# Kernel optimization log

Measured on AMD Instinct MI355X. Metric: run time of the kernel, lower is better.

## Reference

```python
import jax, jax.numpy as jnp
import numpy as np

N_NODES = 100000
N_EDGES = 1250000
D_IN = 64
D_OUT = 64


def setup_inputs() -> dict:
    key = jax.random.key(0)
    k1, k2, k3, k4, k5 = jax.random.split(key, 5)
    x = jax.random.normal(k1, (N_NODES, D_IN), dtype=jnp.float32)
    edge_index = jax.random.randint(k2, (2, N_EDGES), 0, N_NODES, dtype=jnp.int64)
    # Linear weights stored torch-style as [out, in]
    w_neigh = jax.random.normal(k3, (D_OUT, D_IN), dtype=jnp.float32) / np.sqrt(D_IN)
    w_self = jax.random.normal(k4, (D_OUT, D_IN), dtype=jnp.float32) / np.sqrt(D_IN)
    b_self = jax.random.normal(k5, (D_OUT,), dtype=jnp.float32) * 0.01
    return {"x": x, "edge_index": edge_index, "w_neigh": w_neigh, "w_self": w_self, "b_self": b_self}


def reference(x, edge_index, w_neigh, w_self, b_self):
    num_nodes = x.shape[0]
    src, dst = edge_index[0], edge_index[1]
    # mean aggregation of neighbor features: scatter-add then divide by in-degree
    agg = jax.ops.segment_sum(x[src], dst, num_segments=num_nodes)  # [N, d]
    degree = jax.ops.segment_sum(jnp.ones_like(dst, dtype=x.dtype), dst, num_segments=num_nodes)
    degree = jnp.maximum(degree, 1.0)
    agg = agg / degree[:, None]
    return agg @ w_neigh.T + x @ w_self.T + b_self
```

## Files before the change

### kernel.cpp

```cpp
#include <hip/hip_runtime.h>

#define N_NODES 100000
#define N_EDGES 1250000
#define D 64
#define BSH 6
#define BNODES 64
#define NB 1563
#define WSW 68
#define G 512
#define CHUNK 2444
#define MM_BLOCKS ((N_NODES + 127) / 128)
#define BIN_BLOCKS 128
#define BIN_CHUNK ((N_EDGES + BIN_BLOCKS - 1) / BIN_BLOCKS)

typedef unsigned int u32;
typedef short bf16x8 __attribute__((ext_vector_type(8)));
typedef float f32x4 __attribute__((ext_vector_type(4)));

__device__ __forceinline__ u32 pack_bf16(float lo, float hi) {
    u32 a = __float_as_uint(lo);
    u32 b = __float_as_uint(hi);
    a = (a + 0x7fffu + ((a >> 16) & 1u)) >> 16;
    b = (b + 0x7fffu + ((b >> 16) & 1u)) >> 16;
    return a | (b << 16);
}

__global__ void __launch_bounds__(256) k_histw(const int* __restrict__ ei,
                                               u32* __restrict__ ghist,
                                               const float* __restrict__ wn,
                                               const float* __restrict__ wsf,
                                               u32* __restrict__ bfrag) {
    __shared__ u32 hist[NB];
    int tid = threadIdx.x;
    if (blockIdx.x < G) {
        int g = blockIdx.x;
        int e0 = g * CHUNK, e1 = min(e0 + CHUNK, N_EDGES);
        for (int i = tid; i < NB; i += 256) hist[i] = 0;
        __syncthreads();
        const int4* dp = (const int4*)(ei + N_EDGES + e0);
        int nv = (e1 - e0) >> 2;
        for (int i = tid; i < nv; i += 256) {
            int4 d4 = dp[i];
            atomicAdd(&hist[d4.x >> BSH], 1u);
            atomicAdd(&hist[d4.y >> BSH], 1u);
            atomicAdd(&hist[d4.z >> BSH], 1u);
            atomicAdd(&hist[d4.w >> BSH], 1u);
        }
        __syncthreads();
        for (int i = tid; i < NB; i += 256)
            ghist[(size_t)i * G + g] = hist[i];
    } else {
        for (int i = tid; i < 4096; i += 256) {
            int t = i >> 9, h = (i >> 8) & 1, l = (i >> 2) & 63, q = i & 3;
            int k0 = h * 32 + (l >> 4) * 8 + 2 * q;
            int n = t * 16 + (l & 15);
            const float* w = (n < 64) ? &wn[(size_t)n * 64] : &wsf[(size_t)(n - 64) * 64];
            bfrag[i] = pack_bf16(w[k0], w[k0 + 1]);
        }
    }
}

__global__ void __launch_bounds__(512) k_scanB(const u32* __restrict__ ghist,
                                               u32* __restrict__ gbase,
                                               u32* __restrict__ bcnt) {
    __shared__ u32 wt[8];
    int t = threadIdx.x;
    int b = blockIdx.x;
    int lane = t & 63, wv = t >> 6;
    u32 v = ghist[(size_t)b * G + t];
    u32 s = v;
#pragma unroll
    for (int off = 1; off < 64; off <<= 1) {
        u32 n = __shfl_up(s, off, 64);
        if (lane >= off) s += n;
    }
    if (lane == 63) wt[wv] = s;
    __syncthreads();
    u32 add = 0;
#pragma unroll
    for (int q = 0; q < 8; ++q) add += (q < wv) ? wt[q] : 0u;
    u32 incl = s + add;
    gbase[(size_t)b * G + t] = incl - v;
    if (t == G - 1) bcnt[b] = incl;
}

__global__ void __launch_bounds__(256) k_scatmm(const int* __restrict__ ei,
                                                const u32* __restrict__ gbase,
                                                u32* __restrict__ binned,
                                                int cap,
                                                const float* __restrict__ x,
                                                const u32* __restrict__ bfrag,
                                                const float* __restrict__ bias,
                                                u32* __restrict__ y16,
                                                float* __restrict__ zout) {
    __shared__ u32 cur[NB];
    int tid = threadIdx.x;
    if (blockIdx.x < G) {
        int g = blockIdx.x;
        int e0 = g * CHUNK, e1 = min(e0 + CHUNK, N_EDGES);
        for (int i = tid; i < NB; i += 256)
            cur[i] = gbase[(size_t)i * G + g];
        __syncthreads();
        const int4* sp = (const int4*)(ei + e0);
        const int4* dp = (const int4*)(ei + N_EDGES + e0);
        int nv = (e1 - e0) >> 2;
        for (int i = tid; i < nv; i += 256) {
            int4 s4 = sp[i];
            int4 d4 = dp[i];
            int ss[4] = {s4.x, s4.y, s4.z, s4.w};
            int dd[4] = {d4.x, d4.y, d4.z, d4.w};
#pragma unroll
            for (int u = 0; u < 4; ++u) {
                int b = dd[u] >> BSH;
                u32 loc = atomicAdd(&cur[b], 1u);
                if (loc < (u32)cap)
                    binned[(size_t)b * cap + loc] = ((u32)ss[u] << BSH) | (u32)(dd[u] & (BNODES - 1));
            }
        }
        return;
    }

    int w = tid >> 6, l = tid & 63;
    int lg = l >> 4, c = l & 15;
    int nodebase = (blockIdx.x - G) * 128 + w * 32;

    union FU { uint4 u; bf16x8 v; };

    bf16x8 af[2][2];
#pragma unroll
    for (int m = 0; m < 2; ++m) {
        int node = nodebase + m * 16 + c;
        if (node >= N_NODES) node = N_NODES - 1;
        const float4* xr = (const float4*)(x + (size_t)node * D);
#pragma unroll
        for (int h = 0; h < 2; ++h) {
            float4 p0 = xr[h * 8 + lg * 2];
            float4 p1 = xr[h * 8 + lg * 2 + 1];
            FU au;
            au.u.x = pack_bf16(p0.x, p0.y);
            au.u.y = pack_bf16(p0.z, p0.w);
            au.u.z = pack_bf16(p1.x, p1.y);
            au.u.w = pack_bf16(p1.z, p1.w);
            af[m][h] = au.v;
        }
    }

    f32x4 acc[2][8];
#pragma unroll
    for (int m = 0; m < 2; ++m) {
#pragma unroll
        for (int t = 0; t < 4; ++t) acc[m][t] = (f32x4){0.f, 0.f, 0.f, 0.f};
#pragma unroll
        for (int t = 4; t < 8; ++t) {
            float bb = bias[(t - 4) * 16 + c];
            acc[m][t] = (f32x4){bb, bb, bb, bb};
        }
    }

    const uint4* bp = (const uint4*)bfrag;
#pragma unroll
    for (int tc = 0; tc < 2; ++tc) {
        bf16x8 bf[4][2];
#pragma unroll
        for (int tt = 0; tt < 4; ++tt)
#pragma unroll
            for (int h = 0; h < 2; ++h) {
                FU bu;
                bu.u = bp[(((tc * 4 + tt) * 2 + h) * 64) + l];
                bf[tt][h] = bu.v;
            }
#pragma unroll
        for (int m = 0; m < 2; ++m)
#pragma unroll
            for (int tt = 0; tt < 4; ++tt) {
                int t = tc * 4 + tt;
                acc[m][t] = __builtin_amdgcn_mfma_f32_16x16x32_bf16(
                    af[m][0], bf[tt][0], acc[m][t], 0, 0, 0);
                acc[m][t] = __builtin_amdgcn_mfma_f32_16x16x32_bf16(
                    af[m][1], bf[tt][1], acc[m][t], 0, 0, 0);
            }
    }

#pragma unroll
    for (int m = 0; m < 2; ++m) {
        int rowbase = nodebase + m * 16 + lg * 4;
#pragma unroll
        for (int r = 0; r < 4; ++r) {
            int node = rowbase + r;
            bool ok = node < N_NODES;
#pragma unroll
            for (int t = 4; t < 8; ++t) {
                if (ok) zout[(size_t)node * D + (t - 4) * 16 + c] = acc[m][t][r];
            }
#pragma unroll
            for (int t = 0; t < 4; ++t) {
                float v = acc[m][t][r];
                float o = __shfl_xor(v, 1);
                if (ok && !(c & 1))
                    y16[(size_t)node * 32 + t * 8 + (c >> 1)] = pack_bf16(v, o);
            }
        }
    }
}

__global__ void __launch_bounds__(256) k_sort(u32* __restrict__ binned,
                                              const u32* __restrict__ bcnt,
                                              int cap,
                                              uint2* __restrict__ meta) {
    __shared__ u32 eh[1024];
    __shared__ u32 hist[BNODES];
    __shared__ u32 cur[BNODES];
    int tid = threadIdx.x;
    int b = blockIdx.x;
    int cnt = min((int)bcnt[b], cap);
    u32* seg = binned + (size_t)b * cap;

    if (tid < BNODES) hist[tid] = 0;
    __syncthreads();
    const uint4* segv = (const uint4*)seg;
    int nv = cnt >> 2;
    for (int i = tid; i < nv; i += 256) {
        uint4 w4 = segv[i];
        *(uint4*)&eh[4 * i] = w4;
        atomicAdd(&hist[w4.x & (BNODES - 1)], 1u);
        atomicAdd(&hist[w4.y & (BNODES - 1)], 1u);
        atomicAdd(&hist[w4.z & (BNODES - 1)], 1u);
        atomicAdd(&hist[w4.w & (BNODES - 1)], 1u);
    }
    for (int i = (cnt & ~3) + tid; i < cnt; i += 256) {
        u32 w = seg[i];
        eh[i] = w;
        atomicAdd(&hist[w & (BNODES - 1)], 1u);
    }
    __syncthreads();
    if (tid < BNODES) {
        u32 v = hist[tid];
        u32 s = v;
#pragma unroll
        for (int off = 1; off < 64; off <<= 1) {
            u32 n = __shfl_up(s, off, 64);
            if (tid >= off) s += n;
        }
        u32 excl = s - v;
        cur[tid] = excl;
        int node = (b << BSH) + tid;
        if (node < N_NODES)
            meta[node] = make_uint2((u32)((size_t)b * cap + excl), v);
    }
    __syncthreads();
    for (int i = tid; i < cnt; i += 256) {
        u32 w = eh[i];
        u32 p = atomicAdd(&cur[w & (BNODES - 1)], 1u);
        seg[p] = w >> BSH;
    }
}

__global__ void __launch_bounds__(256) k_gather_yz(const u32* __restrict__ y16,
                                                   const u32* __restrict__ binned,
                                                   const uint2* __restrict__ meta,
                                                   float* __restrict__ io) {
    int tid = blockIdx.x * 256 + threadIdx.x;
    int node = tid >> 6;
    if (node >= N_NODES) return;
    int lane = threadIdx.x & 63;
    int sub = lane >> 4;
    int pr = lane & 15;
    const uint2* yv = (const uint2*)y16;
    uint2 m = meta[node];
    u32 o0 = m.x, dg = m.y;

    u32 myidx = 0;
    if (lane < (int)dg) myidx = binned[o0 + lane];

    float a0 = 0.f, a1 = 0.f, a2 = 0.f, a3 = 0.f;
    u32 dmain = min(dg, 64u);
    for (u32 r = 0; r < dmain; r += 32) {
        uint2 w[8];
#pragma unroll
        for (int t = 0; t < 8; ++t) {
            u32 e = r + 4 * t + sub;
            u32 idx = (u32)__shfl((int)myidx, (int)(e & 63));
            w[t] = make_uint2(0u, 0u);
            if (e < dmain) w[t] = yv[(size_t)idx * 16 + pr];
        }
#pragma unroll
        for (int t = 0; t < 8; ++t) {
            if (r + 4u * (u32)t < dmain) {
                a0 += __uint_as_float(w[t].x << 16);
                a1 += __uint_as_float(w[t].x & 0xffff0000u);
                a2 += __uint_as_float(w[t].y << 16);
                a3 += __uint_as_float(w[t].y & 0xffff0000u);
            }
        }
    }
    for (u32 j = o0 + 64; j < o0 + dg; j += 16) {
#pragma unroll
        for (int t = 0; t < 4; ++t) {
            u32 ie = j + 4 * t + sub;
            if (ie < o0 + dg) {
                u32 idx = binned[ie];
                uint2 w = yv[(size_t)idx * 16 + pr];
                a0 += __uint_as_float(w.x << 16);
                a1 += __uint_as_float(w.x & 0xffff0000u);
                a2 += __uint_as_float(w.y << 16);
                a3 += __uint_as_float(w.y & 0xffff0000u);
            }
        }
    }

    a0 += __shfl_xor(a0, 16); a1 += __shfl_xor(a1, 16);
    a2 += __shfl_xor(a2, 16); a3 += __shfl_xor(a3, 16);
    a0 += __shfl_xor(a0, 32); a1 += __shfl_xor(a1, 32);
    a2 += __shfl_xor(a2, 32); a3 += __shfl_xor(a3, 32);
    if (sub == 0) {
        float inv = 1.0f / (float)max(dg, 1u);
        float4 z = *(const float4*)&io[(size_t)node * D + 4 * pr];
        *(float4*)&io[(size_t)node * D + 4 * pr] =
            make_float4(z.x + a0 * inv, z.y + a1 * inv, z.z + a2 * inv, z.w + a3 * inv);
    }
}

__global__ void __launch_bounds__(256) k_bin2(const int* __restrict__ ei,
                                              u32* __restrict__ bcnt,
                                              u32* __restrict__ binned,
                                              int cap) {
    __shared__ u32 hist[NB];
    __shared__ u32 rbase[NB];
    int tid = threadIdx.x;
    int e0 = blockIdx.x * BIN_CHUNK;
    int e1 = min(e0 + BIN_CHUNK, N_EDGES);
    const int* dstp = ei + N_EDGES;
    for (int i = tid; i < NB; i += 256) hist[i] = 0;
    __syncthreads();
    for (int e = e0 + tid; e < e1; e += 256)
        atomicAdd(&hist[dstp[e] >> BSH], 1u);
    __syncthreads();
    for (int i = tid; i < NB; i += 256) {
        u32 h = hist[i];
        rbase[i] = h ? atomicAdd(&bcnt[i], h) : 0u;
        hist[i] = 0;
    }
    __syncthreads();
    for (int e = e0 + tid; e < e1; e += 256) {
        int d = dstp[e];
        int s = ei[e];
        int b = d >> BSH;
        u32 loc = atomicAdd(&hist[b], 1u);
        u32 slot = rbase[b] + loc;
        if (slot < (u32)cap)
            binned[(size_t)b * cap + slot] = ((u32)s << BSH) | (u32)(d & (BNODES - 1));
    }
}

__global__ void __launch_bounds__(256) k_sort_fb(u32* __restrict__ binned,
                                                 const u32* __restrict__ bcnt,
                                                 int cap,
                                                 u32* __restrict__ offs,
                                                 u32* __restrict__ deg) {
    __shared__ u32 eh[1024];
    __shared__ u32 hist[BNODES];
    __shared__ u32 cur[BNODES];
    int tid = threadIdx.x;
    int b = blockIdx.x;
    int cnt = min((int)bcnt[b], cap);
    u32* seg = binned + (size_t)b * cap;
    if (tid < BNODES) hist[tid] = 0;
    __syncthreads();
    for (int i = tid; i < cnt; i += 256) {
        u32 w = seg[i];
        eh[i] = w;
        atomicAdd(&hist[w & (BNODES - 1)], 1u);
    }
    __syncthreads();
    if (tid < BNODES) {
        u32 v = hist[tid];
        u32 s = v;
#pragma unroll
        for (int off = 1; off < 64; off <<= 1) {
            u32 n = __shfl_up(s, off, 64);
            if (tid >= off) s += n;
        }
        u32 excl = s - v;
        cur[tid] = excl;
        int node = (b << BSH) + tid;
        if (node < N_NODES) {
            offs[node] = (u32)((size_t)b * cap + excl);
            deg[node] = v;
        }
    }
    __syncthreads();
    for (int i = tid; i < cnt; i += 256) {
        u32 w = eh[i];
        u32 p = atomicAdd(&cur[w & (BNODES - 1)], 1u);
        seg[p] = w >> BSH;
    }
}

__global__ void __launch_bounds__(256) k_gather32(const float* __restrict__ x,
                                                  const u32* __restrict__ binned,
                                                  const u32* __restrict__ offs,
                                                  const u32* __restrict__ deg,
                                                  float* __restrict__ agg) {
    int tid = blockIdx.x * 256 + threadIdx.x;
    int node = tid >> 6;
    int d = tid & 63;
    if (node >= N_NODES) return;
    u32 o0 = offs[node], dg = deg[node];
    u32 o1 = o0 + dg;
    float s = 0.f;
    u32 j = o0;
    for (; j + 8 <= o1; j += 8) {
        u32 e[8];
        float v[8];
#pragma unroll
        for (int t = 0; t < 8; ++t) e[t] = binned[j + t];
#pragma unroll
        for (int t = 0; t < 8; ++t) v[t] = x[(size_t)e[t] * D + d];
#pragma unroll
        for (int t = 0; t < 8; ++t) s += v[t];
    }
    for (; j < o1; ++j) s += x[(size_t)binned[j] * D + d];
    agg[(size_t)node * D + d] = s / (float)max(dg, 1u);
}

__global__ void __launch_bounds__(256) k_gemm_fb(const float* __restrict__ x,
                                                 const float* __restrict__ wn,
                                                 const float* __restrict__ wsf,
                                                 const float* __restrict__ bias,
                                                 float* __restrict__ io) {
    __shared__ float At[BNODES * WSW];
    __shared__ float Wt[128 * WSW];
    int tid = threadIdx.x;
    int base = blockIdx.x * 64;
    const float4* iop = (const float4*)io;
    const float4* xp  = (const float4*)x;
    for (int i = tid; i < 4096; i += 256) {
        int d = i >> 6, k = i & 63;
        Wt[k * WSW + d] = wn[i];
        Wt[(64 + k) * WSW + d] = wsf[i];
    }
    for (int i = tid; i < 1024; i += 256) {
        int r = i >> 4, q = i & 15;
        int node = base + r;
        float4 v = make_float4(0.f, 0.f, 0.f, 0.f);
        if (node < N_NODES) v = iop[(size_t)node * 16 + q];
        *(float4*)&At[r * WSW + q * 4] = v;
    }
    __syncthreads();
    int tn = tid >> 4, td = tid & 15;
    int n0 = tn * 4, d0 = td * 4;
    float4 b4 = *(const float4*)&bias[d0];
    float acc[4][4];
#pragma unroll
    for (int i = 0; i < 4; ++i) {
        acc[i][0] = b4.x; acc[i][1] = b4.y; acc[i][2] = b4.z; acc[i][3] = b4.w;
    }
#pragma unroll 8
    for (int kc = 0; kc < 16; ++kc) {
        float4 a[4], w[4];
#pragma unroll
        for (int i = 0; i < 4; ++i) a[i] = *(const float4*)&At[(n0 + i) * WSW + kc * 4];
#pragma unroll
        for (int t = 0; t < 4; ++t) w[t] = *(const float4*)&Wt[(kc * 4 + t) * WSW + d0];
#pragma unroll
        for (int i = 0; i < 4; ++i) {
            const float av[4] = {a[i].x, a[i].y, a[i].z, a[i].w};
#pragma unroll
            for (int t = 0; t < 4; ++t) {
                acc[i][0] += av[t] * w[t].x; acc[i][1] += av[t] * w[t].y;
                acc[i][2] += av[t] * w[t].z; acc[i][3] += av[t] * w[t].w;
            }
        }
    }
    __syncthreads();
    for (int i = tid; i < 1024; i += 256) {
        int r = i >> 4, q = i & 15;
        int node = base + r;
        float4 v = make_float4(0.f, 0.f, 0.f, 0.f);
        if (node < N_NODES) v = xp[(size_t)node * 16 + q];
        *(float4*)&At[r * WSW + q * 4] = v;
    }
    __syncthreads();
#pragma unroll 8
    for (int kc = 0; kc < 16; ++kc) {
        float4 a[4], w[4];
#pragma unroll
        for (int i = 0; i < 4; ++i) a[i] = *(const float4*)&At[(n0 + i) * WSW + kc * 4];
#pragma unroll
        for (int t = 0; t < 4; ++t) w[t] = *(const float4*)&Wt[(64 + kc * 4 + t) * WSW + d0];
#pragma unroll
        for (int i = 0; i < 4; ++i) {
            const float av[4] = {a[i].x, a[i].y, a[i].z, a[i].w};
#pragma unroll
            for (int t = 0; t < 4; ++t) {
                acc[i][0] += av[t] * w[t].x; acc[i][1] += av[t] * w[t].y;
                acc[i][2] += av[t] * w[t].z; acc[i][3] += av[t] * w[t].w;
            }
        }
    }
#pragma unroll
    for (int i = 0; i < 4; ++i) {
        int node = base + n0 + i;
        if (node < N_NODES) {
            *(float4*)&io[(size_t)node * D + d0] =
                make_float4(acc[i][0], acc[i][1], acc[i][2], acc[i][3]);
        }
    }
}

extern "C" void kernel_launch(void* const* d_in, const int* in_sizes, int n_in,
                              void* d_out, int out_size, void* d_ws, size_t ws_size,
                              hipStream_t stream) {
    const float* x = (const float*)d_in[0];
    const int* ei = (const int*)d_in[1];
    const float* wn = (const float*)d_in[2];
    const float* wsf = (const float*)d_in[3];
    const float* bias = (const float*)d_in[4];
    float* out = (float*)d_out;

    u32* metaw = (u32*)d_ws;
    u32* bcnt = metaw + 2 * N_NODES;
    u32* bfrag = bcnt + ((NB + 15) & ~15);
    u32* y16 = bfrag + 8192;
    const size_t Y16W = (size_t)N_NODES * (D / 2);
    u32* binned = y16 + Y16W;
    u32* ghist = binned + (size_t)NB * 1024;
    u32* gbase = ghist + (size_t)NB * G;
    size_t fixed = 2 * (size_t)N_NODES + ((NB + 15) & ~15) + 8192;
    size_t need = fixed + Y16W + (size_t)NB * 1024 + 2 * (size_t)NB * G;

    if (ws_size / 4 >= need) {
        const int cap = 1024;
        k_histw<<<G + 1, 256, 0, stream>>>(ei, ghist, wn, wsf, bfrag);
        k_scanB<<<NB, 512, 0, stream>>>(ghist, gbase, bcnt);
        k_scatmm<<<G + MM_BLOCKS, 256, 0, stream>>>(ei, gbase, binned, cap,
                                                    x, bfrag, bias, y16, out);
        k_sort<<<NB, 256, 0, stream>>>(binned, bcnt, cap, (uint2*)metaw);
        k_gather_yz<<<(N_NODES * 64) / 256, 256, 0, stream>>>(y16, binned, (const uint2*)metaw, out);
    } else {
        u32* offs = metaw;
        u32* deg = offs + N_NODES;
        binned = bfrag;
        size_t avail = ws_size / 4 - (fixed - 8192);
        size_t capz = (avail / NB) & ~(size_t)3;
        int cap = (int)(capz < 1024 ? capz : 1024);
        hipMemsetAsync(bcnt, 0, ((NB + 15) & ~15) * sizeof(u32), stream);
        k_bin2<<<BIN_BLOCKS, 256, 0, stream>>>(ei, bcnt, binned, cap);
        k_sort_fb<<<NB, 256, 0, stream>>>(binned, bcnt, cap, offs, deg);
        k_gather32<<<(N_NODES * 64) / 256, 256, 0, stream>>>(x, binned, offs, deg, out);
        k_gemm_fb<<<(N_NODES + 63) / 64, 256, 0, stream>>>(x, wn, wsf, bias, out);
    }
}
```

Measured before the change: 91.18 us.

## Fuse per-bucket sort with neighbor gather into one kernel via LDS

Merges the bucket sort kernel and the gather kernel into a single kernel. Each block sorts its 64-node bucket's edges into shared memory and then has its four waves gather the bf16 projected neighbor rows for 16 nodes each. This removes the write-back of sorted indices and the meta array, the re-read of both, and one kernel launch. The trade-off is far fewer waves in the gather (1563 blocks instead of 25000), which may reduce latency hiding for the random loads, and uses more shared memory per block.

```diff
diff --git a/kernel.cpp b/kernel.cpp
--- a/kernel.cpp
+++ b/kernel.cpp
@@ -203,17 +203,20 @@
     }
 }
 
-__global__ void __launch_bounds__(256) k_sort(u32* __restrict__ binned,
-                                              const u32* __restrict__ bcnt,
-                                              int cap,
-                                              uint2* __restrict__ meta) {
+__global__ void __launch_bounds__(256) k_sortgather(const u32* __restrict__ y16,
+                                                    const u32* __restrict__ binned,
+                                                    const u32* __restrict__ bcnt,
+                                                    int cap,
+                                                    float* __restrict__ io) {
     __shared__ u32 eh[1024];
+    __shared__ u32 srt[1024];
     __shared__ u32 hist[BNODES];
+    __shared__ u32 nbase[BNODES];
     __shared__ u32 cur[BNODES];
     int tid = threadIdx.x;
     int b = blockIdx.x;
     int cnt = min((int)bcnt[b], cap);
-    u32* seg = binned + (size_t)b * cap;
+    const u32* seg = binned + (size_t)b * cap;
 
     if (tid < BNODES) hist[tid] = 0;
     __syncthreads();
@@ -242,81 +245,57 @@
             if (tid >= off) s += n;
         }
         u32 excl = s - v;
+        nbase[tid] = excl;
         cur[tid] = excl;
-        int node = (b << BSH) + tid;
-        if (node < N_NODES)
-            meta[node] = make_uint2((u32)((size_t)b * cap + excl), v);
     }
     __syncthreads();
     for (int i = tid; i < cnt; i += 256) {
         u32 w = eh[i];
         u32 p = atomicAdd(&cur[w & (BNODES - 1)], 1u);
-        seg[p] = w >> BSH;
-    }
-}
-
-__global__ void __launch_bounds__(256) k_gather_yz(const u32* __restrict__ y16,
-                                                   const u32* __restrict__ binned,
-                                                   const uint2* __restrict__ meta,
-                                                   float* __restrict__ io) {
-    int tid = blockIdx.x * 256 + threadIdx.x;
-    int node = tid >> 6;
-    if (node >= N_NODES) return;
-    int lane = threadIdx.x & 63;
+        srt[p] = w >> BSH;
+    }
+    __syncthreads();
+
+    int wv = tid >> 6, lane = tid & 63;
     int sub = lane >> 4;
     int pr = lane & 15;
     const uint2* yv = (const uint2*)y16;
-    uint2 m = meta[node];
-    u32 o0 = m.x, dg = m.y;
-
-    u32 myidx = 0;
-    if (lane < (int)dg) myidx = binned[o0 + lane];
-
-    float a0 = 0.f, a1 = 0.f, a2 = 0.f, a3 = 0.f;
-    u32 dmain = min(dg, 64u);
-    for (u32 r = 0; r < dmain; r += 32) {
-        uint2 w[8];
-#pragma unroll
-        for (int t = 0; t < 8; ++t) {
-            u32 e = r + 4 * t + sub;
-            u32 idx = (u32)__shfl((int)myidx, (int)(e & 63));
-            w[t] = make_uint2(0u, 0u);
-            if (e < dmain) w[t] = yv[(size_t)idx * 16 + pr];
-        }
-#pragma unroll
-        for (int t = 0; t < 8; ++t) {
-            if (r + 4u * (u32)t < dmain) {
-                a0 += __uint_as_float(w[t].x << 16);
-                a1 += __uint_as_float(w[t].x & 0xffff0000u);
-                a2 += __uint_as_float(w[t].y << 16);
-                a3 += __uint_as_float(w[t].y & 0xffff0000u);
-            }
-        }
-    }
-    for (u32 j = o0 + 64; j < o0 + dg; j += 16) {
-#pragma unroll
-        for (int t = 0; t < 4; ++t) {
-            u32 ie = j + 4 * t + sub;
-            if (ie < o0 + dg) {
-                u32 idx = binned[ie];
-                uint2 w = yv[(size_t)idx * 16 + pr];
-                a0 += __uint_as_float(w.x << 16);
-                a1 += __uint_as_float(w.x & 0xffff0000u);
-                a2 += __uint_as_float(w.y << 16);
-                a3 += __uint_as_float(w.y & 0xffff0000u);
-            }
-        }
-    }
-
-    a0 += __shfl_xor(a0, 16); a1 += __shfl_xor(a1, 16);
-    a2 += __shfl_xor(a2, 16); a3 += __shfl_xor(a3, 16);
-    a0 += __shfl_xor(a0, 32); a1 += __shfl_xor(a1, 32);
-    a2 += __shfl_xor(a2, 32); a3 += __shfl_xor(a3, 32);
-    if (sub == 0) {
-        float inv = 1.0f / (float)max(dg, 1u);
-        float4 z = *(const float4*)&io[(size_t)node * D + 4 * pr];
-        *(float4*)&io[(size_t)node * D + 4 * pr] =
-            make_float4(z.x + a0 * inv, z.y + a1 * inv, z.z + a2 * inv, z.w + a3 * inv);
+    int nodebase = b << BSH;
+
+    for (int i = 0; i < 16; ++i) {
+        int dl = wv * 16 + i;
+        int node = nodebase + dl;
+        u32 o0 = nbase[dl];
+        u32 dg = hist[dl];
+        float a0 = 0.f, a1 = 0.f, a2 = 0.f, a3 = 0.f;
+        for (u32 r = 0; r < dg; r += 32) {
+            uint2 w[8];
+#pragma unroll
+            for (int t = 0; t < 8; ++t) {
+                u32 e = r + 4 * t + sub;
+                w[t] = make_uint2(0u, 0u);
+                if (e < dg) w[t] = yv[(size_t)srt[o0 + e] * 16 + pr];
+            }
+#pragma unroll
+            for (int t = 0; t < 8; ++t) {
+                if (r + 4u * (u32)t < dg) {
+                    a0 += __uint_as_float(w[t].x << 16);
+                    a1 += __uint_as_float(w[t].x & 0xffff0000u);
+                    a2 += __uint_as_float(w[t].y << 16);
+                    a3 += __uint_as_float(w[t].y & 0xffff0000u);
+                }
+            }
+        }
+        a0 += __shfl_xor(a0, 16); a1 += __shfl_xor(a1, 16);
+        a2 += __shfl_xor(a2, 16); a3 += __shfl_xor(a3, 16);
+        a0 += __shfl_xor(a0, 32); a1 += __shfl_xor(a1, 32);
+        a2 += __shfl_xor(a2, 32); a3 += __shfl_xor(a3, 32);
+        if (sub == 0 && node < N_NODES) {
+            float inv = 1.0f / (float)max(dg, 1u);
+            float4 z = *(const float4*)&io[(size_t)node * D + 4 * pr];
+            *(float4*)&io[(size_t)node * D + 4 * pr] =
+                make_float4(z.x + a0 * inv, z.y + a1 * inv, z.z + a2 * inv, z.w + a3 * inv);
+        }
     }
 }
 
@@ -518,8 +497,8 @@
     const float* bias = (const float*)d_in[4];
     float* out = (float*)d_out;
 
-    u32* metaw = (u32*)d_ws;
-    u32* bcnt = metaw + 2 * N_NODES;
+    u32* scratch = (u32*)d_ws;
+    u32* bcnt = scratch + 2 * N_NODES;
     u32* bfrag = bcnt + ((NB + 15) & ~15);
     u32* y16 = bfrag + 8192;
     const size_t Y16W = (size_t)N_NODES * (D / 2);
@@ -535,10 +514,9 @@
         k_scanB<<<NB, 512, 0, stream>>>(ghist, gbase, bcnt);
         k_scatmm<<<G + MM_BLOCKS, 256, 0, stream>>>(ei, gbase, binned, cap,
                                                     x, bfrag, bias, y16, out);
-        k_sort<<<NB, 256, 0, stream>>>(binned, bcnt, cap, (uint2*)metaw);
-        k_gather_yz<<<(N_NODES * 64) / 256, 256, 0, stream>>>(y16, binned, (const uint2*)metaw, out);
+        k_sortgather<<<NB, 256, 0, stream>>>(y16, binned, bcnt, cap, out);
     } else {
-        u32* offs = metaw;
+        u32* offs = scratch;
         u32* deg = offs + N_NODES;
         binned = bfrag;
         size_t avail = ws_size / 4 - (fixed - 8192);
```

New measurement: 83.64 us. 8.3% less time.
